# Kernel optimization log

Measured on AMD Instinct MI355X. Metric: run time of the kernel, lower is better.

Reference implementation:

```python
import jax, jax.numpy as jnp
import numpy as np

NUM_PT = 13
NUM_SQ = 64
SQPT = NUM_SQ * NUM_PT            # 832
NUM_FEATURES = NUM_SQ * SQPT      # 53248
ATTN_TABLE = NUM_SQ * SQPT * SQPT # 44302336
DEPTH = 256
DFF = 1024
NUM_HEADS = 4
N = 512
LN_EPS = 1e-5


def layer_norm(x, w, b):
    m = jnp.mean(x, axis=-1, keepdims=True)
    v = jnp.mean(jnp.square(x - m), axis=-1, keepdims=True)
    return (x - m) * jax.lax.rsqrt(v + LN_EPS) * w + b


def setup_inputs() -> dict:
    key = jax.random.key(0)
    ks = jax.random.split(key, 12)
    # indices must satisfy piece_indices = ksq*832 + offset, offset in [0,832)
    pno = jax.random.randint(ks[0], (N, NUM_SQ), 0, SQPT, dtype=jnp.int32)
    ksq = jax.random.randint(ks[1], (N,), 0, NUM_SQ, dtype=jnp.int32)
    piece_indices = ksq[:, None] * SQPT + pno
    attn_bias_indices = jax.random.randint(ks[2], (N, NUM_SQ * NUM_SQ), 0, NUM_PT * NUM_PT, dtype=jnp.int32)
    f32 = jnp.float32
    return {
        "piece_indices": piece_indices,
        "attn_bias_indices": attn_bias_indices,
        "ksq": ksq,
        "value_table": jax.random.normal(ks[3], (NUM_FEATURES, DEPTH), f32) * 0.02,
        "attn_weights_table": jax.random.normal(ks[4], (ATTN_TABLE, NUM_HEADS), f32) * 0.02,
        "attn_bias_table": jax.random.normal(ks[5], (NUM_PT * NUM_PT, NUM_HEADS), f32) * 0.02,
        "attn_scale": jnp.asarray(100.0, f32),
        "W1": jax.random.normal(ks[6], (DEPTH, DFF), f32) * 0.02,
        "b1": jnp.zeros((DFF,), f32),
        "W2": jax.random.normal(ks[7], (DFF, DEPTH), f32) * 0.02,
        "b2": jnp.zeros((DEPTH,), f32),
        "ln1_w": jnp.ones((DEPTH,), f32),
        "ln1_b": jnp.zeros((DEPTH,), f32),
        "ln2_w": jnp.ones((DEPTH,), f32),
        "ln2_b": jnp.zeros((DEPTH,), f32),
    }


def reference(piece_indices, attn_bias_indices, ksq, value_table, attn_weights_table,
              attn_bias_table, attn_scale, W1, b1, W2, b2, ln1_w, ln1_b, ln2_w, ln2_b):
    n = piece_indices.shape[0]
    dh = DEPTH // NUM_HEADS
    pno = piece_indices - ksq[:, None] * SQPT                      # [N,64] in [0,832)
    attn_idx = (pno[:, :, None] * SQPT + pno[:, None, :]
                + ksq[:, None, None] * SQPT * SQPT)                # [N,64,64]
    aw = attn_weights_table[attn_idx]                              # [N,64,64,H]
    abi = attn_bias_indices.reshape(n, NUM_SQ, NUM_SQ).transpose(0, 2, 1)
    ab = attn_bias_table[abi]                                      # [N,64,64,H]
    logits = ((aw + ab) * attn_scale).transpose(0, 3, 1, 2)        # [N,H,64,64]
    attn = jax.nn.softmax(logits, axis=-1)
    values = value_table[piece_indices].reshape(n, NUM_SQ, NUM_HEADS, dh).transpose(0, 2, 1, 3)  # [N,H,64,dh]
    ctx = jnp.einsum('nhqk,nhkd->nhqd', attn, values) + values
    x = layer_norm(ctx.transpose(0, 2, 1, 3).reshape(n, NUM_SQ, DEPTH), ln1_w, ln1_b)
    ffn = jnp.maximum(x @ W1 + b1, 0.0) @ W2 + b2
    return layer_norm(ffn + x, ln2_w, ln2_b)
```

## Files before the change

### kernel.cpp

```cpp
#include <hip/hip_runtime.h>
#include <stdint.h>

typedef unsigned short u16;
typedef __attribute__((ext_vector_type(8))) short bf16x8;
typedef __attribute__((ext_vector_type(4))) float f32x4;

typedef __attribute__((address_space(1))) const unsigned char gas_u8;
typedef __attribute__((address_space(3))) unsigned char las_u8;

__device__ __forceinline__ void gload_lds16(const void* g, void* l) {
  __builtin_amdgcn_global_load_lds((const gas_u8*)g, (las_u8*)l, 16, 0, 0);
}

__device__ __forceinline__ u16 f2bf(float f) {
  uint32_t u = __float_as_uint(f);
  u += 0x7fffu + ((u >> 16) & 1u);
  return (u16)(u >> 16);
}
__device__ __forceinline__ float bf2f(u16 v) {
  return __uint_as_float(((uint32_t)v) << 16);
}

__global__ __launch_bounds__(256, 4)
void transpose_kernel(const float* __restrict__ W1, u16* __restrict__ W1T,
                      const float* __restrict__ W2, u16* __restrict__ W2T) {
  __shared__ u16 tile[64 * 66];
  int b = blockIdx.x;
  const float* src; u16* dst; int R, C, tc, tr;
  if (b < 64) { src = W1; dst = W1T; R = 256; C = 1024; tc = (b & 15) * 64; tr = (b >> 4) * 64; }
  else { b -= 64; src = W2; dst = W2T; R = 1024; C = 256; tc = (b & 3) * 64; tr = (b >> 2) * 64; }
  const int t = threadIdx.x;
  const int c = t & 63, rb = t >> 6;
#pragma unroll
  for (int i = 0; i < 16; ++i) {
    int r = i * 4 + rb;
    tile[r * 66 + c] = f2bf(src[(size_t)(tr + r) * C + tc + c]);
  }
  __syncthreads();
#pragma unroll
  for (int i = 0; i < 16; ++i) {
    int x = i * 4 + rb;
    int y = c;
    dst[(size_t)(tc + x) * R + tr + y] = tile[y * 66 + x];
  }
}

#define SM_BASE 65536
#define OFF_ABT  (SM_BASE + 0)
#define OFF_PNO  (SM_BASE + 2704)
#define OFF_PIDX (SM_BASE + 2960)
#define OFF_REDA (SM_BASE + 3216)
#define OFF_REDB (SM_BASE + 7312)
#define OFF_RED  (SM_BASE + 11408)
#define OFF_HB   (SM_BASE + 0)

__global__ __launch_bounds__(256, 2)
void mega_kernel(const int* __restrict__ piece_indices,
                 const int* __restrict__ abi_idx,
                 const int* __restrict__ ksq,
                 const float* __restrict__ value_table,
                 const float* __restrict__ aw_table,
                 const float* __restrict__ ab_table,
                 const float* __restrict__ scale_p,
                 const float* __restrict__ ln1w, const float* __restrict__ ln1b,
                 const u16* __restrict__ W1T, const u16* __restrict__ W2T,
                 const float* __restrict__ b1, const float* __restrict__ b2,
                 const float* __restrict__ ln2w, const float* __restrict__ ln2b,
                 float* __restrict__ out) {
  __shared__ __align__(16) char SMEM[79872];
  u16* VT = (u16*)(SMEM);
  u16* P  = (u16*)(SMEM + 32768);
  float* abt_s = (float*)(SMEM + OFF_ABT);
  int* pno_s   = (int*)(SMEM + OFF_PNO);
  int* pidx_s  = (int*)(SMEM + OFF_PIDX);
  float* redA  = (float*)(SMEM + OFF_REDA);
  float* redB  = (float*)(SMEM + OFF_REDB);
  float* red   = (float*)(SMEM + OFF_RED);

  const int n = blockIdx.x;
  const int t = threadIdx.x;
  const int h = t >> 6;
  const int lane = t & 63;
  const int ks = ksq[n];

  if (t < 64) {
    int pi = piece_indices[n * 64 + t];
    pidx_s[t] = pi;
    pno_s[t] = pi - ks * 832;
  }
  for (int i = t; i < 676; i += 256) abt_s[i] = ab_table[i];
  __syncthreads();

  const float scale = scale_p[0];
  const int q = lane, kg = h;

  {
    const int base = ks * (832 * 832);
#pragma unroll
    for (int j = 0; j < 16; ++j) {
      int qj = h * 16 + j;
      int kk = lane ^ qj;
      int idx = base + pno_s[qj] * 832 + pno_s[kk];
      gload_lds16(aw_table + (size_t)idx * 4, SMEM + qj * 1024);
    }
  }
  __syncthreads();

  bf16x8 vreg[8];
  {
    const int feat = t;
#pragma unroll
    for (int c = 0; c < 8; ++c) {
      float tmp[8];
#pragma unroll
      for (int jj = 0; jj < 8; ++jj)
        tmp[jj] = value_table[(size_t)pidx_s[c * 8 + jj] * 256 + feat];
#pragma unroll
      for (int jj = 0; jj < 8; ++jj) vreg[c][jj] = (short)f2bf(tmp[jj]);
    }
  }

  float l[4][16];
#pragma unroll
  for (int j = 0; j < 16; ++j) {
    int k = kg * 16 + j;
    f32x4 aw4 = *(const f32x4*)(SMEM + q * 1024 + ((k ^ q) << 4));
    int bi = abi_idx[n * 4096 + k * 64 + q];
    f32x4 ab4 = *(const f32x4*)(abt_s + bi * 4);
#pragma unroll
    for (int hh = 0; hh < 4; ++hh) l[hh][j] = (aw4[hh] + ab4[hh]) * scale;
  }

  float mkg[4];
#pragma unroll
  for (int hh = 0; hh < 4; ++hh) {
    float m = l[hh][0];
#pragma unroll
    for (int j = 1; j < 16; ++j) m = fmaxf(m, l[hh][j]);
    float s = 0.f;
#pragma unroll
    for (int j = 0; j < 16; ++j) { l[hh][j] = __expf(l[hh][j] - m); s += l[hh][j]; }
    mkg[hh] = m;
    redA[(kg * 4 + hh) * 64 + q] = m;
    redB[(kg * 4 + hh) * 64 + q] = s;
  }
  __syncthreads();
  float adj[4];
#pragma unroll
  for (int hh = 0; hh < 4; ++hh) {
    float m0 = redA[(0 * 4 + hh) * 64 + q], m1 = redA[(1 * 4 + hh) * 64 + q];
    float m2 = redA[(2 * 4 + hh) * 64 + q], m3 = redA[(3 * 4 + hh) * 64 + q];
    float m = fmaxf(fmaxf(m0, m1), fmaxf(m2, m3));
    float s = redB[(0 * 4 + hh) * 64 + q] * __expf(m0 - m) +
              redB[(1 * 4 + hh) * 64 + q] * __expf(m1 - m) +
              redB[(2 * 4 + hh) * 64 + q] * __expf(m2 - m) +
              redB[(3 * 4 + hh) * 64 + q] * __expf(m3 - m);
    adj[hh] = __expf(mkg[hh] - m) / s;
  }

#pragma unroll
  for (int hh = 0; hh < 4; ++hh) {
#pragma unroll
    for (int c2 = 0; c2 < 2; ++c2) {
      int c = kg * 2 + c2;
      bf16x8 pv;
#pragma unroll
      for (int j8 = 0; j8 < 8; ++j8) {
        int j = c2 * 8 + j8;
        int k = kg * 16 + j;
        float v = l[hh][j] * adj[hh] + ((k == q) ? 1.f : 0.f);
        pv[j8] = (short)f2bf(v);
      }
      int off = (hh * 64 + q) * 64 + ((c ^ (q & 7)) << 3);
      *(bf16x8*)(&P[off]) = pv;
    }
  }
  {
    const int feat = t;
#pragma unroll
    for (int c = 0; c < 8; ++c) {
      int off = feat * 64 + ((c ^ (feat & 7)) << 3);
      *(bf16x8*)(&VT[off]) = vreg[c];
    }
  }
  __syncthreads();

  const int li = lane & 15, lg = lane >> 4;
  f32x4 acc[4][4] = {};
#pragma unroll
  for (int kst = 0; kst < 2; ++kst) {
    int cg = kst * 4 + lg;
    bf16x8 aF[4], bF[4];
#pragma unroll
    for (int mi = 0; mi < 4; ++mi) {
      int row = mi * 16 + li;
      aF[mi] = *(const bf16x8*)(&P[(h * 64 + row) * 64 + ((cg ^ (row & 7)) << 3)]);
    }
#pragma unroll
    for (int ni = 0; ni < 4; ++ni) {
      int rr = h * 64 + ni * 16 + li;
      bF[ni] = *(const bf16x8*)(&VT[rr * 64 + ((cg ^ (rr & 7)) << 3)]);
    }
#pragma unroll
    for (int mi = 0; mi < 4; ++mi)
#pragma unroll
      for (int ni = 0; ni < 4; ++ni)
        acc[mi][ni] = __builtin_amdgcn_mfma_f32_16x16x32_bf16(aF[mi], bF[ni], acc[mi][ni], 0, 0, 0);
  }

#pragma unroll
  for (int mi = 0; mi < 4; ++mi)
#pragma unroll
    for (int r = 0; r < 4; ++r) {
      float s1 = 0.f, s2 = 0.f;
#pragma unroll
      for (int ni = 0; ni < 4; ++ni) { float v = acc[mi][ni][r]; s1 += v; s2 += v * v; }
#pragma unroll
      for (int mk = 1; mk < 16; mk <<= 1) { s1 += __shfl_xor(s1, mk, 64); s2 += __shfl_xor(s2, mk, 64); }
      if (li == 0) { int q2 = mi * 16 + lg * 4 + r; red[(h * 64 + q2) * 2 + 0] = s1; red[(h * 64 + q2) * 2 + 1] = s2; }
    }
  __syncthreads();

  u16* Xl = (u16*)(SMEM + 32768);
  {
    float w_[4], b_[4];
#pragma unroll
    for (int ni = 0; ni < 4; ++ni) {
      int f = h * 64 + ni * 16 + li;
      w_[ni] = ln1w[f]; b_[ni] = ln1b[f];
    }
#pragma unroll
    for (int mi = 0; mi < 4; ++mi)
#pragma unroll
      for (int r = 0; r < 4; ++r) {
        int q2 = mi * 16 + lg * 4 + r;
        float S1 = red[(0 * 64 + q2) * 2] + red[(1 * 64 + q2) * 2] +
                   red[(2 * 64 + q2) * 2] + red[(3 * 64 + q2) * 2];
        float S2 = red[(0 * 64 + q2) * 2 + 1] + red[(1 * 64 + q2) * 2 + 1] +
                   red[(2 * 64 + q2) * 2 + 1] + red[(3 * 64 + q2) * 2 + 1];
        float mean = S1 * (1.f / 256.f);
        float var = S2 * (1.f / 256.f) - mean * mean;
        float rs = rsqrtf(var + 1e-5f);
#pragma unroll
        for (int ni = 0; ni < 4; ++ni) {
          int col = h * 64 + ni * 16 + li;
          float xv = (acc[mi][ni][r] - mean) * rs * w_[ni] + b_[ni];
          int cc = col >> 3;
          *(u16*)((char*)Xl + q2 * 512 + (((cc ^ (q2 & 7)) & 31) << 4) + (col & 7) * 2) = f2bf(xv);
        }
      }
  }

  u16* Wb = (u16*)(SMEM);
  u16* Hb = (u16*)(SMEM + OFF_HB);
  const int wv = h;
  f32x4 oacc[4][4] = {};

  for (int ch = 0; ch < 16; ++ch) {
#pragma unroll
    for (int it = 0; it < 8; ++it) {
      int idx = it * 256 + t;
      int row = idx >> 5, c = idx & 31;
      const u16* g = W1T + (size_t)(ch * 64 + row) * 256 + (((c ^ (row & 7)) & 31) << 3);
      gload_lds16(g, (char*)Wb + it * 4096 + wv * 1024);
    }
    __syncthreads();

    f32x4 hacc[4] = {};
#pragma unroll
    for (int kst = 0; kst < 8; ++kst) {
      int cg = kst * 4 + lg;
      bf16x8 aF[4], bF;
      {
        int brow = wv * 16 + li;
        bF = *(const bf16x8*)((char*)Wb + brow * 512 + (((cg ^ (brow & 7)) & 31) << 4));
      }
#pragma unroll
      for (int mi = 0; mi < 4; ++mi) {
        int row = mi * 16 + li;
        aF[mi] = *(const bf16x8*)((char*)Xl + row * 512 + (((cg ^ (row & 7)) & 31) << 4));
      }
#pragma unroll
      for (int mi = 0; mi < 4; ++mi)
        hacc[mi] = __builtin_amdgcn_mfma_f32_16x16x32_bf16(aF[mi], bF, hacc[mi], 0, 0, 0);
    }
    __syncthreads();

    {
      float bv = b1[ch * 64 + wv * 16 + li];
      int col = wv * 16 + li;
      int c2 = col >> 3;
#pragma unroll
      for (int mi = 0; mi < 4; ++mi)
#pragma unroll
        for (int r = 0; r < 4; ++r) {
          int row = mi * 16 + lg * 4 + r;
          float v = fmaxf(hacc[mi][r] + bv, 0.f);
          *(u16*)((char*)Hb + row * 128 + ((c2 ^ (row & 7)) << 4) + (col & 7) * 2) = f2bf(v);
        }
    }
#pragma unroll
    for (int it = 0; it < 8; ++it) {
      int idx = it * 256 + t;
      int row = idx >> 3, c = idx & 7;
      const u16* g = W2T + (size_t)row * 1024 + ch * 64 + ((c ^ (row & 7)) << 3);
      gload_lds16(g, (char*)Wb + it * 4096 + wv * 1024);
    }
    __syncthreads();

#pragma unroll
    for (int kst = 0; kst < 2; ++kst) {
      int cg = kst * 4 + lg;
      bf16x8 aF[4], bF[4];
#pragma unroll
      for (int mi = 0; mi < 4; ++mi) {
        int row = mi * 16 + li;
        aF[mi] = *(const bf16x8*)((char*)Hb + row * 128 + (((cg ^ (row & 7)) & 7) << 4));
      }
#pragma unroll
      for (int ni = 0; ni < 4; ++ni) {
        int row = wv * 64 + ni * 16 + li;
        bF[ni] = *(const bf16x8*)((char*)Wb + row * 128 + (((cg ^ (row & 7)) & 7) << 4));
      }
#pragma unroll
      for (int mi = 0; mi < 4; ++mi)
#pragma unroll
        for (int ni = 0; ni < 4; ++ni)
          oacc[mi][ni] = __builtin_amdgcn_mfma_f32_16x16x32_bf16(aF[mi], bF[ni], oacc[mi][ni], 0, 0, 0);
    }
    __syncthreads();
  }

  float bias2[4];
#pragma unroll
  for (int ni = 0; ni < 4; ++ni) bias2[ni] = b2[wv * 64 + ni * 16 + li];

#pragma unroll
  for (int mi = 0; mi < 4; ++mi)
#pragma unroll
    for (int r = 0; r < 4; ++r) {
      float s1 = 0.f, s2 = 0.f;
      int row = mi * 16 + lg * 4 + r;
#pragma unroll
      for (int ni = 0; ni < 4; ++ni) {
        int col = wv * 64 + ni * 16 + li;
        int cc = col >> 3;
        u16 xres = *(const u16*)((char*)Xl + row * 512 + (((cc ^ (row & 7)) & 31) << 4) + (col & 7) * 2);
        float v = oacc[mi][ni][r] + bias2[ni] + bf2f(xres);
        oacc[mi][ni][r] = v;
        s1 += v; s2 += v * v;
      }
#pragma unroll
      for (int mk = 1; mk < 16; mk <<= 1) { s1 += __shfl_xor(s1, mk, 64); s2 += __shfl_xor(s2, mk, 64); }
      if (li == 0) { int q2 = mi * 16 + lg * 4 + r; red[(wv * 64 + q2) * 2 + 0] = s1; red[(wv * 64 + q2) * 2 + 1] = s2; }
    }
  __syncthreads();

  float lw[4], lb[4];
#pragma unroll
  for (int ni = 0; ni < 4; ++ni) {
    int col = wv * 64 + ni * 16 + li;
    lw[ni] = ln2w[col]; lb[ni] = ln2b[col];
  }
#pragma unroll
  for (int mi = 0; mi < 4; ++mi)
#pragma unroll
    for (int r = 0; r < 4; ++r) {
      int q2 = mi * 16 + lg * 4 + r;
      float S1 = red[(0 * 64 + q2) * 2] + red[(1 * 64 + q2) * 2] +
                 red[(2 * 64 + q2) * 2] + red[(3 * 64 + q2) * 2];
      float S2 = red[(0 * 64 + q2) * 2 + 1] + red[(1 * 64 + q2) * 2 + 1] +
                 red[(2 * 64 + q2) * 2 + 1] + red[(3 * 64 + q2) * 2 + 1];
      float mean = S1 * (1.f / 256.f);
      float var = S2 * (1.f / 256.f) - mean * mean;
      float rs = rsqrtf(var + 1e-5f);
      size_t rbase = (size_t)(n * 64 + q2) * 256;
#pragma unroll
      for (int ni = 0; ni < 4; ++ni)
        out[rbase + wv * 64 + ni * 16 + li] = (oacc[mi][ni][r] - mean) * rs * lw[ni] + lb[ni];
    }
}

extern "C" void kernel_launch(void* const* d_in, const int* in_sizes, int n_in,
                              void* d_out, int out_size, void* d_ws, size_t ws_size,
                              hipStream_t stream) {
  const int* piece_indices = (const int*)d_in[0];
  const int* abi_idx       = (const int*)d_in[1];
  const int* ksq           = (const int*)d_in[2];
  const float* value_table = (const float*)d_in[3];
  const float* aw_table    = (const float*)d_in[4];
  const float* ab_table    = (const float*)d_in[5];
  const float* attn_scale  = (const float*)d_in[6];
  const float* W1          = (const float*)d_in[7];
  const float* b1          = (const float*)d_in[8];
  const float* W2          = (const float*)d_in[9];
  const float* b2          = (const float*)d_in[10];
  const float* ln1w        = (const float*)d_in[11];
  const float* ln1b        = (const float*)d_in[12];
  const float* ln2w        = (const float*)d_in[13];
  const float* ln2b        = (const float*)d_in[14];

  char* ws = (char*)d_ws;
  u16* W1T = (u16*)(ws);
  u16* W2T = (u16*)(ws + (512 << 10));
  float* out = (float*)d_out;

  transpose_kernel<<<128, 256, 0, stream>>>(W1, W1T, W2, W2T);
  mega_kernel<<<512, 256, 0, stream>>>(piece_indices, abi_idx, ksq, value_table,
                                       aw_table, ab_table, attn_scale, ln1w, ln1b,
                                       W1T, W2T, b1, b2, ln2w, ln2b, out);
}
```

Measured before the change: 110.9 us.

## Read FFN weights directly from global into MFMA fragments, widen hidden chunks

The FFN loop no longer stages W1/W2 tiles into LDS with global_load_lds. Each wave now loads its B fragments straight from global memory (L2-resident bf16 weights) and processes 256-wide hidden chunks over 4 iterations instead of 64-wide chunks over 16, holding a 4x4 tile of hidden accumulators. This removes LDS staging traffic and many barriers. The abi index loads are also hoisted ahead of the barrier so they overlap the attention-weight gather. The trade-offs are more accumulator registers and global-load latency sitting directly in front of the MFMAs.

```diff
diff --git a/kernel.cpp b/kernel.cpp
--- a/kernel.cpp
+++ b/kernel.cpp
@@ -52,7 +52,6 @@
 #define OFF_REDA (SM_BASE + 3216)
 #define OFF_REDB (SM_BASE + 7312)
 #define OFF_RED  (SM_BASE + 11408)
-#define OFF_HB   (SM_BASE + 0)
 
 __global__ __launch_bounds__(256, 2)
 void mega_kernel(const int* __restrict__ piece_indices,
@@ -104,7 +103,6 @@
       gload_lds16(aw_table + (size_t)idx * 4, SMEM + qj * 1024);
     }
   }
-  __syncthreads();
 
   bf16x8 vreg[8];
   {
@@ -119,14 +117,19 @@
       for (int jj = 0; jj < 8; ++jj) vreg[c][jj] = (short)f2bf(tmp[jj]);
     }
   }
+  int bi[16];
+#pragma unroll
+  for (int j = 0; j < 16; ++j)
+    bi[j] = abi_idx[n * 4096 + (kg * 16 + j) * 64 + q];
+
+  __syncthreads();
 
   float l[4][16];
 #pragma unroll
   for (int j = 0; j < 16; ++j) {
     int k = kg * 16 + j;
     f32x4 aw4 = *(const f32x4*)(SMEM + q * 1024 + ((k ^ q) << 4));
-    int bi = abi_idx[n * 4096 + k * 64 + q];
-    f32x4 ab4 = *(const f32x4*)(abt_s + bi * 4);
+    f32x4 ab4 = *(const f32x4*)(abt_s + bi[j] * 4);
 #pragma unroll
     for (int hh = 0; hh < 4; ++hh) l[hh][j] = (aw4[hh] + ab4[hh]) * scale;
   }
@@ -250,30 +253,22 @@
         }
       }
   }
-
-  u16* Wb = (u16*)(SMEM);
-  u16* Hb = (u16*)(SMEM + OFF_HB);
+  __syncthreads();
+
+  u16* Hb2 = (u16*)(SMEM);
   const int wv = h;
   f32x4 oacc[4][4] = {};
 
-  for (int ch = 0; ch < 16; ++ch) {
-#pragma unroll
-    for (int it = 0; it < 8; ++it) {
-      int idx = it * 256 + t;
-      int row = idx >> 5, c = idx & 31;
-      const u16* g = W1T + (size_t)(ch * 64 + row) * 256 + (((c ^ (row & 7)) & 31) << 3);
-      gload_lds16(g, (char*)Wb + it * 4096 + wv * 1024);
-    }
-    __syncthreads();
-
-    f32x4 hacc[4] = {};
+  for (int ch = 0; ch < 4; ++ch) {
+    f32x4 hacc[4][4] = {};
 #pragma unroll
     for (int kst = 0; kst < 8; ++kst) {
       int cg = kst * 4 + lg;
-      bf16x8 aF[4], bF;
-      {
-        int brow = wv * 16 + li;
-        bF = *(const bf16x8*)((char*)Wb + brow * 512 + (((cg ^ (brow & 7)) & 31) << 4));
+      bf16x8 aF[4], bF[4];
+#pragma unroll
+      for (int ni = 0; ni < 4; ++ni) {
+        int brow = ch * 256 + wv * 64 + ni * 16 + li;
+        bF[ni] = *(const bf16x8*)(W1T + (size_t)brow * 256 + cg * 8);
       }
 #pragma unroll
       for (int mi = 0; mi < 4; ++mi) {
@@ -282,45 +277,41 @@
       }
 #pragma unroll
       for (int mi = 0; mi < 4; ++mi)
-        hacc[mi] = __builtin_amdgcn_mfma_f32_16x16x32_bf16(aF[mi], bF, hacc[mi], 0, 0, 0);
+#pragma unroll
+        for (int ni = 0; ni < 4; ++ni)
+          hacc[mi][ni] = __builtin_amdgcn_mfma_f32_16x16x32_bf16(aF[mi], bF[ni], hacc[mi][ni], 0, 0, 0);
     }
     __syncthreads();
 
-    {
-      float bv = b1[ch * 64 + wv * 16 + li];
-      int col = wv * 16 + li;
-      int c2 = col >> 3;
+#pragma unroll
+    for (int ni = 0; ni < 4; ++ni) {
+      int col = wv * 64 + ni * 16 + li;
+      float bv = b1[ch * 256 + col];
+      int cc = col >> 3;
 #pragma unroll
       for (int mi = 0; mi < 4; ++mi)
 #pragma unroll
         for (int r = 0; r < 4; ++r) {
           int row = mi * 16 + lg * 4 + r;
-          float v = fmaxf(hacc[mi][r] + bv, 0.f);
-          *(u16*)((char*)Hb + row * 128 + ((c2 ^ (row & 7)) << 4) + (col & 7) * 2) = f2bf(v);
+          float v = fmaxf(hacc[mi][ni][r] + bv, 0.f);
+          *(u16*)((char*)Hb2 + row * 512 + (((cc ^ (row & 7)) & 31) << 4) + (col & 7) * 2) = f2bf(v);
         }
     }
-#pragma unroll
-    for (int it = 0; it < 8; ++it) {
-      int idx = it * 256 + t;
-      int row = idx >> 3, c = idx & 7;
-      const u16* g = W2T + (size_t)row * 1024 + ch * 64 + ((c ^ (row & 7)) << 3);
-      gload_lds16(g, (char*)Wb + it * 4096 + wv * 1024);
-    }
     __syncthreads();
 
 #pragma unroll
-    for (int kst = 0; kst < 2; ++kst) {
+    for (int kst = 0; kst < 8; ++kst) {
       int cg = kst * 4 + lg;
       bf16x8 aF[4], bF[4];
 #pragma unroll
+      for (int ni = 0; ni < 4; ++ni) {
+        int orow = wv * 64 + ni * 16 + li;
+        bF[ni] = *(const bf16x8*)(W2T + (size_t)orow * 1024 + ch * 256 + cg * 8);
+      }
+#pragma unroll
       for (int mi = 0; mi < 4; ++mi) {
         int row = mi * 16 + li;
-        aF[mi] = *(const bf16x8*)((char*)Hb + row * 128 + (((cg ^ (row & 7)) & 7) << 4));
-      }
-#pragma unroll
-      for (int ni = 0; ni < 4; ++ni) {
-        int row = wv * 64 + ni * 16 + li;
-        bF[ni] = *(const bf16x8*)((char*)Wb + row * 128 + (((cg ^ (row & 7)) & 7) << 4));
+        aF[mi] = *(const bf16x8*)((char*)Hb2 + row * 512 + (((cg ^ (row & 7)) & 31) << 4));
       }
 #pragma unroll
       for (int mi = 0; mi < 4; ++mi)
@@ -328,7 +319,6 @@
         for (int ni = 0; ni < 4; ++ni)
           oacc[mi][ni] = __builtin_amdgcn_mfma_f32_16x16x32_bf16(aF[mi], bF[ni], oacc[mi][ni], 0, 0, 0);
     }
-    __syncthreads();
   }
 
   float bias2[4];
```

Result: slower. 138.7 us (+25.1%).
